# Kernel tuning notes

Measured on AMD Instinct MI355X. Metric: run time of the kernel, lower is better.

The kernel has to match this reference:

```python
import jax, jax.numpy as jnp
import numpy as np
from jax import lax

B, CI, CO, H, W = 2, 256, 256, 128, 128
K = 3
K2 = K * K  # 9 kernel taps
BN_EPS = 1e-5


def setup_inputs() -> dict:
    key = jax.random.key(0)
    ks = jax.random.split(key, 9)
    x = jax.random.normal(ks[0], (B, CI, H, W), jnp.float32)
    # conv_offset_mask: Conv2d(chi, 3*K2, 3, stride=1, pad=1) -> [o_y/o_x interleaved (2*K2) | mask (K2)]
    w_off = jax.random.normal(ks[1], (3 * K2, CI, K, K), jnp.float32) * 0.01
    b_off = jax.random.normal(ks[2], (3 * K2,), jnp.float32) * 0.01
    # modulated deformable conv weight/bias
    w_dcn = jax.random.normal(ks[3], (CO, CI, K, K), jnp.float32) * (1.0 / np.float32(np.sqrt(CI * K2)))
    b_dcn = jax.random.normal(ks[4], (CO,), jnp.float32) * 0.01
    # BatchNorm2d (eval-mode affine + running stats)
    gamma = jax.random.uniform(ks[5], (CO,), jnp.float32, 0.5, 1.5)
    beta = jax.random.normal(ks[6], (CO,), jnp.float32) * 0.1
    run_mean = jax.random.normal(ks[7], (CO,), jnp.float32) * 0.1
    run_var = jax.random.uniform(ks[8], (CO,), jnp.float32, 0.5, 1.5)
    return {"x": x, "w_off": w_off, "b_off": b_off, "w_dcn": w_dcn,
            "b_dcn": b_dcn, "gamma": gamma, "beta": beta,
            "run_mean": run_mean, "run_var": run_var}


def _bilinear(x, py, px):
    """Sample x [B,C,H,W] at fractional coords (py,px) [B,H,W]; zero outside."""
    Bx, C, Hx, Wx = x.shape
    y0 = jnp.floor(py)
    x0 = jnp.floor(px)
    ly = py - y0
    lx = px - x0
    xf = x.reshape(Bx, C, Hx * Wx)

    def gather(yy, xx):
        valid = ((yy >= 0) & (yy <= Hx - 1) & (xx >= 0) & (xx <= Wx - 1)).astype(x.dtype)
        yi = jnp.clip(yy, 0, Hx - 1).astype(jnp.int32)
        xi = jnp.clip(xx, 0, Wx - 1).astype(jnp.int32)
        idx = (yi * Wx + xi).reshape(Bx, 1, Hx * Wx)
        v = jnp.take_along_axis(xf, idx, axis=2).reshape(Bx, C, Hx, Wx)
        return v * valid[:, None]

    w00 = ((1 - ly) * (1 - lx))[:, None]
    w01 = ((1 - ly) * lx)[:, None]
    w10 = (ly * (1 - lx))[:, None]
    w11 = (ly * lx)[:, None]
    return (w00 * gather(y0, x0) + w01 * gather(y0, x0 + 1)
            + w10 * gather(y0 + 1, x0) + w11 * gather(y0 + 1, x0 + 1))


def _deform_conv_bn_relu(x, w_off, b_off, w_dcn, b_dcn, gamma, beta, run_mean, run_var):
    # offset/mask predictor conv (stride 1, pad 1)
    om = lax.conv_general_dilated(x, w_off, (1, 1), ((1, 1), (1, 1))) + b_off[None, :, None, None]
    dy = om[:, 0:2 * K2:2]          # [B,K2,H,W]
    dx = om[:, 1:2 * K2:2]          # [B,K2,H,W]
    mask = jax.nn.sigmoid(om[:, 2 * K2:])  # [B,K2,H,W] modulation

    hh = jnp.arange(H, dtype=x.dtype)[:, None]  # [H,1]
    ww = jnp.arange(W, dtype=x.dtype)[None, :]  # [1,W]

    out = jnp.zeros((x.shape[0], w_dcn.shape[0], H, W), x.dtype)
    for k in range(K2):  # fixed small loop over the 9 kernel taps
        i, j = k // K, k % K
        py = hh - 1 + i + dy[:, k]  # pad=1, dilation=1
        px = ww - 1 + j + dx[:, k]
        val = _bilinear(x, py, px) * mask[:, k][:, None]  # [B,CI,H,W]
        out = out + jnp.einsum('oc,bchw->bohw', w_dcn[:, :, i, j], val)
    out = out + b_dcn[None, :, None, None]

    # BatchNorm2d (eval mode) + ReLU
    inv = gamma / jnp.sqrt(run_var + BN_EPS)
    out = out * inv[None, :, None, None] + (beta - run_mean * inv)[None, :, None, None]
    return jnp.maximum(out, 0.0)


def reference(x, w_off, b_off, w_dcn, b_dcn, gamma, beta, run_mean, run_var):
    return _deform_conv_bn_relu(x, w_off, b_off, w_dcn, b_dcn, gamma, beta, run_mean, run_var)
```

## Files before the change

### kernel.cpp

```cpp
#include <hip/hip_runtime.h>
#include <math.h>

#define Bn 2
#define CIc 256
#define COc 256
#define Hh 128
#define Ww 128
#define HW (Hh*Ww)

typedef unsigned short u16;
typedef unsigned int u32;
typedef __bf16 bf16x8 __attribute__((ext_vector_type(8)));
typedef float  f32x4  __attribute__((ext_vector_type(4)));
typedef float  f32x2  __attribute__((ext_vector_type(2)));
typedef u32    u32x4v __attribute__((ext_vector_type(4)));

#define WOFP_OFF  0
#define WPACK_OFF 36864
#define SCALE_OFF 331776
#define SHIFT_OFF 332032
#define XT_OFF    332288

__device__ __forceinline__ u16 f2bf(float f) {
    u32 u = __builtin_bit_cast(u32, f);
    return (u16)((u + 0x7FFFu + ((u >> 16) & 1u)) >> 16);
}
__device__ __forceinline__ u32 pkbf(float lo, float hi) {
    __bf16 a = (__bf16)lo, b = (__bf16)hi;
    return (u32)__builtin_bit_cast(u16, a) | ((u32)__builtin_bit_cast(u16, b) << 16);
}
__device__ __forceinline__ f32x2 unpk(u32 u) {
    f32x2 r;
    r.x = __builtin_bit_cast(float, u << 16);
    r.y = __builtin_bit_cast(float, u & 0xFFFF0000u);
    return r;
}

__global__ void prep_kernel(const float* __restrict__ w_off,
                            const float* __restrict__ w_dcn,
                            const float* __restrict__ b_dcn,
                            const float* __restrict__ gamma,
                            const float* __restrict__ beta,
                            const float* __restrict__ rmean,
                            const float* __restrict__ rvar,
                            float* __restrict__ ws) {
    int tid = blockIdx.x*blockDim.x + threadIdx.x;
    int nth = gridDim.x*blockDim.x;
    u16* wofp = (u16*)(ws + WOFP_OFF);
    u16* wpk  = (u16*)(ws + WPACK_OFF);
    for (int idx = tid; idx < 9*8*32*4*8; idx += nth) {
        int j = idx & 7, kb = (idx>>3)&3, co = (idx>>5)&31, s = (idx>>10)&7, k = idx>>13;
        int ci = kb*64 + s*8 + j;
        float v = (co < 27) ? w_off[(co*CIc + ci)*9 + k] : 0.f;
        wofp[idx] = f2bf(v);
    }
    for (int idx = tid; idx < 9*8*256*4*8; idx += nth) {
        int j = idx & 7, kb = (idx>>3)&3, co = (idx>>5)&255, s = (idx>>13)&7, k = idx>>16;
        int ci = kb*64 + s*8 + j;
        wpk[idx] = f2bf(w_dcn[(co*CIc + ci)*9 + k]);
    }
    if (tid < COc) {
        float inv = gamma[tid] * rsqrtf(rvar[tid] + 1e-5f);
        ws[SCALE_OFF+tid] = inv;
        ws[SHIFT_OFF+tid] = beta[tid] - rmean[tid]*inv + b_dcn[tid]*inv;
    }
}

__global__ __launch_bounds__(256) void transpose_kernel(const float* __restrict__ x,
                                                        float* __restrict__ ws) {
    __shared__ float tile[256][33];
    int bid = blockIdx.x;
    int b   = bid >> 9;
    int pxt = bid & 511;
    const float* xb = x + (size_t)b*CIc*HW + pxt*32;
    int px = threadIdx.x & 31, cg = threadIdx.x >> 5;
    #pragma unroll 8
    for (int it = 0; it < 32; it++) {
        int ci = it*8 + cg;
        tile[ci][px] = xb[(size_t)ci*HW + px];
    }
    __syncthreads();
    int px2 = threadIdx.x >> 3, oct = threadIdx.x & 7;
    u16* xto = (u16*)(ws + XT_OFF) + (((size_t)b*HW + pxt*32 + px2) << 8);
    #pragma unroll
    for (int uu = 0; uu < 4; uu++) {
        int u = uu*8 + oct;
        int cib = (u & 3)*64 + (u >> 2)*8;
        u32x4v v;
        #pragma unroll
        for (int t = 0; t < 4; t++)
            v[t] = pkbf(tile[cib + 2*t][px2], tile[cib + 2*t + 1][px2]);
        *(u32x4v*)(xto + u*8) = v;
    }
}

__device__ __forceinline__ void calc_corners(const float* spy, const float* spxs, const float* smk,
        int k, int p_s, int sub, const u16* xt,
        float& w00, float& w01, float& w10, float& w11,
        const u16*& x00, const u16*& x01, const u16*& x10, const u16*& x11) {
    float pyv = spy[k*64 + p_s], pxv = spxs[k*64 + p_s], mv = smk[k*64 + p_s];
    float y0f = floorf(pyv), x0f = floorf(pxv);
    float ly = pyv - y0f, lx = pxv - x0f;
    int y0 = (int)y0f, x0i = (int)x0f;
    int y1 = y0 + 1, x1i = x0i + 1;
    float wy0 = ((unsigned)y0  < Hh) ? (1.f-ly) : 0.f;
    float wy1 = ((unsigned)y1  < Hh) ? ly       : 0.f;
    float wx0 = ((unsigned)x0i < Ww) ? (1.f-lx) : 0.f;
    float wx1 = ((unsigned)x1i < Ww) ? lx       : 0.f;
    w00 = wy0*wx0*mv; w01 = wy0*wx1*mv; w10 = wy1*wx0*mv; w11 = wy1*wx1*mv;
    int cy0 = min(max(y0,0),Hh-1), cy1 = min(max(y1,0),Hh-1);
    int cx0 = min(max(x0i,0),Ww-1), cx1 = min(max(x1i,0),Ww-1);
    x00 = xt + ((((cy0<<7)+cx0)<<8) + sub*8);
    x01 = xt + ((((cy0<<7)+cx1)<<8) + sub*8);
    x10 = xt + ((((cy1<<7)+cx0)<<8) + sub*8);
    x11 = xt + ((((cy1<<7)+cx1)<<8) + sub*8);
}

__global__ __launch_bounds__(256, 2) void fused_kernel(const float* __restrict__ b_off,
                                                       const float* __restrict__ ws,
                                                       float* __restrict__ out) {
    __shared__ __align__(16) char smem[65536 + 3*576*4];
    float* fin  = (float*)smem;
    float* spy  = (float*)(smem + 65536);
    float* spxs = spy + 576;
    float* smk  = spxs + 576;

    int tid = threadIdx.x;
    int bid = blockIdx.x;
    int tile = (bid & 7)*64 + (bid >> 3);
    int b = tile >> 8;
    int pixbase = (tile & 255) * 64;
    int h  = pixbase >> 7;
    int w0 = pixbase & 127;

    const u16* wofp = (const u16*)(ws + WOFP_OFF);
    const u16* wpk  = (const u16*)(ws + WPACK_OFF);
    const u16* xt   = (const u16*)(ws + XT_OFF) + (size_t)b*HW*256;

    int l  = tid & 63;
    int wv = tid >> 6;
    int kb = l >> 4;
    int aoff = (l & 15)*32 + kb*8;
    int pxl = l & 15;

    {
        int pxa = wv*16 + (l & 15);
        f32x4 oa0 = {0.f,0.f,0.f,0.f}, oa1 = {0.f,0.f,0.f,0.f};
        #pragma unroll
        for (int k = 0; k < 9; k++) {
            int ky = k/3, kx = k - 3*ky;
            int y  = h + ky - 1;
            int xw = w0 + pxa + kx - 1;
            bool ok = ((unsigned)y < Hh) && ((unsigned)xw < Ww);
            const u16* brow = xt + (((y << 7) + xw) << 8);
            const u16* wk = wofp + k*8192;
            #pragma unroll
            for (int s = 0; s < 8; s++) {
                bf16x8 bf = {};
                if (ok) bf = *(const bf16x8*)(brow + s*32 + kb*8);
                bf16x8 a0 = *(const bf16x8*)(wk + s*1024 + aoff);
                bf16x8 a1 = *(const bf16x8*)(wk + s*1024 + 512 + aoff);
                oa0 = __builtin_amdgcn_mfma_f32_16x16x32_bf16(a0, bf, oa0, 0,0,0);
                oa1 = __builtin_amdgcn_mfma_f32_16x16x32_bf16(a1, bf, oa1, 0,0,0);
            }
        }
        #pragma unroll
        for (int r = 0; r < 4; r++) {
            fin[(kb*4 + r)*64 + pxa]      = oa0[r];
            fin[(16 + kb*4 + r)*64 + pxa] = oa1[r];
        }
    }
    __syncthreads();
    for (int idx = tid; idx < 576; idx += 256) {
        int k = idx >> 6, p = idx & 63;
        float dy = fin[(2*k)*64 + p]   + b_off[2*k];
        float dx = fin[(2*k+1)*64 + p] + b_off[2*k+1];
        float mv = fin[(18+k)*64 + p]  + b_off[18+k];
        spy[idx]  = (float)(h - 1 + k/3) + dy;
        spxs[idx] = (float)(w0 + p - 1 + k%3) + dx;
        smk[idx]  = 1.f/(1.f + __expf(-mv));
    }
    __syncthreads();

    int p_s = tid >> 2;
    int sub = tid & 3;
    u32 wrbase0 = (u32)p_s*512;
    u32 wsub = (u32)sub << 4;
    u32 wswz = (u32)(p_s & 7) << 4;
    u32 rswz = (u32)(pxl & 7) << 4;

    f32x4 acc[4][4];
    #pragma unroll
    for (int mi = 0; mi < 4; mi++)
        #pragma unroll
        for (int bq = 0; bq < 4; bq++)
            acc[mi][bq] = (f32x4){0.f,0.f,0.f,0.f};

    {
        float w00,w01,w10,w11; const u16 *x00,*x01,*x10,*x11;
        calc_corners(spy, spxs, smk, 0, p_s, sub, xt, w00,w01,w10,w11, x00,x01,x10,x11);
        u32x4v g[4][4];
        #pragma unroll
        for (int hh = 0; hh < 2; hh++) {
            #pragma unroll
            for (int it = 0; it < 4; it++) {
                int o = (hh*4 + it) << 5;
                g[it][0] = *(const u32x4v*)(x00 + o);
                g[it][1] = *(const u32x4v*)(x01 + o);
                g[it][2] = *(const u32x4v*)(x10 + o);
                g[it][3] = *(const u32x4v*)(x11 + o);
            }
            #pragma unroll
            for (int it = 0; it < 4; it++) {
                u32x4v vv;
                #pragma unroll
                for (int w2 = 0; w2 < 4; w2++) {
                    f32x2 r = unpk(g[it][0][w2])*w00 + unpk(g[it][1][w2])*w01
                            + unpk(g[it][2][w2])*w10 + unpk(g[it][3][w2])*w11;
                    vv[w2] = pkbf(r.x, r.y);
                }
                u32 uoff = (((u32)(hh*4+it) << 6) | wsub) ^ wswz;
                *(u32x4v*)(smem + wrbase0 + uoff) = vv;
            }
        }
    }
    __syncthreads();

    for (int k = 0; k < 9; k++) {
        const char* base_r = smem + ((k & 1) << 15);
        char* base_w = smem + (((k + 1) & 1) << 15);
        const u16* wkbase = wpk + k*65536 + wv*2048 + aoff;

        float w00,w01,w10,w11; const u16 *x00=xt,*x01=xt,*x10=xt,*x11=xt;
        bool stage = (k != 8);
        if (stage)
            calc_corners(spy, spxs, smk, k+1, p_s, sub, xt, w00,w01,w10,w11, x00,x01,x10,x11);

        u32x4v g[4][4];
        if (stage) {
            #pragma unroll
            for (int it = 0; it < 4; it++) {
                int o = it << 5;
                g[it][0] = *(const u32x4v*)(x00 + o);
                g[it][1] = *(const u32x4v*)(x01 + o);
                g[it][2] = *(const u32x4v*)(x10 + o);
                g[it][3] = *(const u32x4v*)(x11 + o);
            }
        }
        #pragma unroll
        for (int s = 0; s < 4; s++) {
            const u16* wkk = wkbase + s*8192;
            bf16x8 a0 = *(const bf16x8*)(wkk);
            bf16x8 a1 = *(const bf16x8*)(wkk + 512);
            bf16x8 a2 = *(const bf16x8*)(wkk + 1024);
            bf16x8 a3 = *(const bf16x8*)(wkk + 1536);
            u32 inn = ((u32)(s*64 + kb*16)) ^ rswz;
            #pragma unroll
            for (int bq = 0; bq < 4; bq++) {
                bf16x8 bb = *(const bf16x8*)(base_r + (pxl + bq*16)*512 + inn);
                acc[0][bq] = __builtin_amdgcn_mfma_f32_16x16x32_bf16(a0,bb,acc[0][bq],0,0,0);
                acc[1][bq] = __builtin_amdgcn_mfma_f32_16x16x32_bf16(a1,bb,acc[1][bq],0,0,0);
                acc[2][bq] = __builtin_amdgcn_mfma_f32_16x16x32_bf16(a2,bb,acc[2][bq],0,0,0);
                acc[3][bq] = __builtin_amdgcn_mfma_f32_16x16x32_bf16(a3,bb,acc[3][bq],0,0,0);
            }
        }
        if (stage) {
            #pragma unroll
            for (int it = 0; it < 4; it++) {
                u32x4v vv;
                #pragma unroll
                for (int w2 = 0; w2 < 4; w2++) {
                    f32x2 r = unpk(g[it][0][w2])*w00 + unpk(g[it][1][w2])*w01
                            + unpk(g[it][2][w2])*w10 + unpk(g[it][3][w2])*w11;
                    vv[w2] = pkbf(r.x, r.y);
                }
                u32 uoff = (((u32)it << 6) | wsub) ^ wswz;
                *(u32x4v*)(base_w + wrbase0 + uoff) = vv;
            }
            #pragma unroll
            for (int it = 0; it < 4; it++) {
                int o = (4 + it) << 5;
                g[it][0] = *(const u32x4v*)(x00 + o);
                g[it][1] = *(const u32x4v*)(x01 + o);
                g[it][2] = *(const u32x4v*)(x10 + o);
                g[it][3] = *(const u32x4v*)(x11 + o);
            }
        }
        #pragma unroll
        for (int s = 4; s < 8; s++) {
            const u16* wkk = wkbase + s*8192;
            bf16x8 a0 = *(const bf16x8*)(wkk);
            bf16x8 a1 = *(const bf16x8*)(wkk + 512);
            bf16x8 a2 = *(const bf16x8*)(wkk + 1024);
            bf16x8 a3 = *(const bf16x8*)(wkk + 1536);
            u32 inn = ((u32)(s*64 + kb*16)) ^ rswz;
            #pragma unroll
            for (int bq = 0; bq < 4; bq++) {
                bf16x8 bb = *(const bf16x8*)(base_r + (pxl + bq*16)*512 + inn);
                acc[0][bq] = __builtin_amdgcn_mfma_f32_16x16x32_bf16(a0,bb,acc[0][bq],0,0,0);
                acc[1][bq] = __builtin_amdgcn_mfma_f32_16x16x32_bf16(a1,bb,acc[1][bq],0,0,0);
                acc[2][bq] = __builtin_amdgcn_mfma_f32_16x16x32_bf16(a2,bb,acc[2][bq],0,0,0);
                acc[3][bq] = __builtin_amdgcn_mfma_f32_16x16x32_bf16(a3,bb,acc[3][bq],0,0,0);
            }
        }
        if (stage) {
            #pragma unroll
            for (int it = 0; it < 4; it++) {
                u32x4v vv;
                #pragma unroll
                for (int w2 = 0; w2 < 4; w2++) {
                    f32x2 r = unpk(g[it][0][w2])*w00 + unpk(g[it][1][w2])*w01
                            + unpk(g[it][2][w2])*w10 + unpk(g[it][3][w2])*w11;
                    vv[w2] = pkbf(r.x, r.y);
                }
                u32 uoff = (((u32)(4+it) << 6) | wsub) ^ wswz;
                *(u32x4v*)(base_w + wrbase0 + uoff) = vv;
            }
        }
        __syncthreads();
    }

    int rbase = kb*4;
    #pragma unroll
    for (int mi = 0; mi < 4; mi++) {
        #pragma unroll
        for (int r = 0; r < 4; r++) {
            int co = wv*64 + mi*16 + rbase + r;
            float sc = ws[SCALE_OFF+co], sh = ws[SHIFT_OFF+co];
            float* op = out + ((size_t)(b*COc + co))*HW + pixbase + pxl;
            #pragma unroll
            for (int bq = 0; bq < 4; bq++)
                op[bq*16] = fmaxf(acc[mi][bq][r]*sc + sh, 0.f);
        }
    }
}

extern "C" void kernel_launch(void* const* d_in, const int* in_sizes, int n_in,
                              void* d_out, int out_size, void* d_ws, size_t ws_size,
                              hipStream_t stream) {
    const float* x     = (const float*)d_in[0];
    const float* w_off = (const float*)d_in[1];
    const float* b_off = (const float*)d_in[2];
    const float* w_dcn = (const float*)d_in[3];
    const float* b_dcn = (const float*)d_in[4];
    const float* gamma = (const float*)d_in[5];
    const float* beta  = (const float*)d_in[6];
    const float* rmean = (const float*)d_in[7];
    const float* rvar  = (const float*)d_in[8];
    float* out = (float*)d_out;
    float* ws  = (float*)d_ws;

    prep_kernel<<<512, 256, 0, stream>>>(w_off, w_dcn, b_dcn, gamma, beta, rmean, rvar, ws);
    transpose_kernel<<<1024, 256, 0, stream>>>(x, ws);
    fused_kernel<<<512, 256, 0, stream>>>(b_off, ws, out);
}
```

Baseline: 117.8 us.

## Double fused kernel block to 512 threads, halving per-wave output channels

The fused deformable-conv kernel now runs 8 waves per block instead of 4. Each wave owns 32 output channels instead of 64, so the accumulator register footprint halves, and the launch bound is raised to target more resident waves. The offset-predictor MFMA work and the bilinear gather staging are redistributed so each thread samples 4 chunks instead of 8. The staging loads are also no longer interleaved with the MFMA loop; they are all issued before it. This trades software overlap and weight-register reuse for higher occupancy, but the LDS footprint per block is unchanged, which may limit how many blocks actually co-reside.

```diff
diff --git a/kernel.cpp b/kernel.cpp
--- a/kernel.cpp
+++ b/kernel.cpp
@@ -7,6 +7,7 @@
 #define Hh 128
 #define Ww 128
 #define HW (Hh*Ww)
+#define THREADS 512
 
 typedef unsigned short u16;
 typedef unsigned int u32;
@@ -116,7 +117,7 @@
     x11 = xt + ((((cy1<<7)+cx1)<<8) + sub*8);
 }
 
-__global__ __launch_bounds__(256, 2) void fused_kernel(const float* __restrict__ b_off,
+__global__ __launch_bounds__(512, 4) void fused_kernel(const float* __restrict__ b_off,
                                                        const float* __restrict__ ws,
                                                        float* __restrict__ out) {
     __shared__ __align__(16) char smem[65536 + 3*576*4];
@@ -140,12 +141,13 @@
     int l  = tid & 63;
     int wv = tid >> 6;
     int kb = l >> 4;
-    int aoff = (l & 15)*32 + kb*8;
     int pxl = l & 15;
+    int aoff = pxl*32 + kb*8;
 
     {
-        int pxa = wv*16 + (l & 15);
-        f32x4 oa0 = {0.f,0.f,0.f,0.f}, oa1 = {0.f,0.f,0.f,0.f};
+        int pxa = ((wv >> 1) & 3)*16 + pxl;
+        int coh = wv & 1;
+        f32x4 oa = {0.f,0.f,0.f,0.f};
         #pragma unroll
         for (int k = 0; k < 9; k++) {
             int ky = k/3, kx = k - 3*ky;
@@ -153,25 +155,21 @@
             int xw = w0 + pxa + kx - 1;
             bool ok = ((unsigned)y < Hh) && ((unsigned)xw < Ww);
             const u16* brow = xt + (((y << 7) + xw) << 8);
-            const u16* wk = wofp + k*8192;
+            const u16* wk = wofp + k*8192 + coh*512;
             #pragma unroll
             for (int s = 0; s < 8; s++) {
                 bf16x8 bf = {};
                 if (ok) bf = *(const bf16x8*)(brow + s*32 + kb*8);
                 bf16x8 a0 = *(const bf16x8*)(wk + s*1024 + aoff);
-                bf16x8 a1 = *(const bf16x8*)(wk + s*1024 + 512 + aoff);
-                oa0 = __builtin_amdgcn_mfma_f32_16x16x32_bf16(a0, bf, oa0, 0,0,0);
-                oa1 = __builtin_amdgcn_mfma_f32_16x16x32_bf16(a1, bf, oa1, 0,0,0);
-            }
-        }
-        #pragma unroll
-        for (int r = 0; r < 4; r++) {
-            fin[(kb*4 + r)*64 + pxa]      = oa0[r];
-            fin[(16 + kb*4 + r)*64 + pxa] = oa1[r];
-        }
+                oa = __builtin_amdgcn_mfma_f32_16x16x32_bf16(a0, bf, oa, 0,0,0);
+            }
+        }
+        #pragma unroll
+        for (int r = 0; r < 4; r++)
+            fin[(coh*16 + kb*4 + r)*64 + pxa] = oa[r];
     }
     __syncthreads();
-    for (int idx = tid; idx < 576; idx += 256) {
+    for (int idx = tid; idx < 576; idx += THREADS) {
         int k = idx >> 6, p = idx & 63;
         float dy = fin[(2*k)*64 + p]   + b_off[2*k];
         float dx = fin[(2*k+1)*64 + p] + b_off[2*k+1];
@@ -182,16 +180,16 @@
     }
     __syncthreads();
 
-    int p_s = tid >> 2;
-    int sub = tid & 3;
+    int p_s = tid >> 3;
+    int sub = tid & 7;
     u32 wrbase0 = (u32)p_s*512;
     u32 wsub = (u32)sub << 4;
     u32 wswz = (u32)(p_s & 7) << 4;
     u32 rswz = (u32)(pxl & 7) << 4;
 
-    f32x4 acc[4][4];
+    f32x4 acc[2][4];
     #pragma unroll
-    for (int mi = 0; mi < 4; mi++)
+    for (int mi = 0; mi < 2; mi++)
         #pragma unroll
         for (int bq = 0; bq < 4; bq++)
             acc[mi][bq] = (f32x4){0.f,0.f,0.f,0.f};
@@ -201,120 +199,70 @@
         calc_corners(spy, spxs, smk, 0, p_s, sub, xt, w00,w01,w10,w11, x00,x01,x10,x11);
         u32x4v g[4][4];
         #pragma unroll
-        for (int hh = 0; hh < 2; hh++) {
-            #pragma unroll
-            for (int it = 0; it < 4; it++) {
-                int o = (hh*4 + it) << 5;
-                g[it][0] = *(const u32x4v*)(x00 + o);
-                g[it][1] = *(const u32x4v*)(x01 + o);
-                g[it][2] = *(const u32x4v*)(x10 + o);
-                g[it][3] = *(const u32x4v*)(x11 + o);
-            }
-            #pragma unroll
-            for (int it = 0; it < 4; it++) {
+        for (int t = 0; t < 4; t++) {
+            int o = t << 6;
+            g[t][0] = *(const u32x4v*)(x00 + o);
+            g[t][1] = *(const u32x4v*)(x01 + o);
+            g[t][2] = *(const u32x4v*)(x10 + o);
+            g[t][3] = *(const u32x4v*)(x11 + o);
+        }
+        #pragma unroll
+        for (int t = 0; t < 4; t++) {
+            u32x4v vv;
+            #pragma unroll
+            for (int w2 = 0; w2 < 4; w2++) {
+                f32x2 r = unpk(g[t][0][w2])*w00 + unpk(g[t][1][w2])*w01
+                        + unpk(g[t][2][w2])*w10 + unpk(g[t][3][w2])*w11;
+                vv[w2] = pkbf(r.x, r.y);
+            }
+            u32 uoff = (((u32)t << 7) | wsub) ^ wswz;
+            *(u32x4v*)(smem + wrbase0 + uoff) = vv;
+        }
+    }
+    __syncthreads();
+
+    for (int k = 0; k < 9; k++) {
+        const char* base_r = smem + ((k & 1) << 15);
+        char* base_w = smem + (((k + 1) & 1) << 15);
+        const u16* wkbase = wpk + k*65536 + wv*1024 + aoff;
+
+        if (k != 8) {
+            float w00,w01,w10,w11; const u16 *x00,*x01,*x10,*x11;
+            calc_corners(spy, spxs, smk, k+1, p_s, sub, xt, w00,w01,w10,w11, x00,x01,x10,x11);
+            u32x4v g[4][4];
+            #pragma unroll
+            for (int t = 0; t < 4; t++) {
+                int o = t << 6;
+                g[t][0] = *(const u32x4v*)(x00 + o);
+                g[t][1] = *(const u32x4v*)(x01 + o);
+                g[t][2] = *(const u32x4v*)(x10 + o);
+                g[t][3] = *(const u32x4v*)(x11 + o);
+            }
+            #pragma unroll
+            for (int t = 0; t < 4; t++) {
                 u32x4v vv;
                 #pragma unroll
                 for (int w2 = 0; w2 < 4; w2++) {
-                    f32x2 r = unpk(g[it][0][w2])*w00 + unpk(g[it][1][w2])*w01
-                            + unpk(g[it][2][w2])*w10 + unpk(g[it][3][w2])*w11;
+                    f32x2 r = unpk(g[t][0][w2])*w00 + unpk(g[t][1][w2])*w01
+                            + unpk(g[t][2][w2])*w10 + unpk(g[t][3][w2])*w11;
                     vv[w2] = pkbf(r.x, r.y);
                 }
-                u32 uoff = (((u32)(hh*4+it) << 6) | wsub) ^ wswz;
-                *(u32x4v*)(smem + wrbase0 + uoff) = vv;
-            }
-        }
-    }
-    __syncthreads();
-
-    for (int k = 0; k < 9; k++) {
-        const char* base_r = smem + ((k & 1) << 15);
-        char* base_w = smem + (((k + 1) & 1) << 15);
-        const u16* wkbase = wpk + k*65536 + wv*2048 + aoff;
-
-        float w00,w01,w10,w11; const u16 *x00=xt,*x01=xt,*x10=xt,*x11=xt;
-        bool stage = (k != 8);
-        if (stage)
-            calc_corners(spy, spxs, smk, k+1, p_s, sub, xt, w00,w01,w10,w11, x00,x01,x10,x11);
-
-        u32x4v g[4][4];
-        if (stage) {
-            #pragma unroll
-            for (int it = 0; it < 4; it++) {
-                int o = it << 5;
-                g[it][0] = *(const u32x4v*)(x00 + o);
-                g[it][1] = *(const u32x4v*)(x01 + o);
-                g[it][2] = *(const u32x4v*)(x10 + o);
-                g[it][3] = *(const u32x4v*)(x11 + o);
-            }
-        }
-        #pragma unroll
-        for (int s = 0; s < 4; s++) {
+                u32 uoff = (((u32)t << 7) | wsub) ^ wswz;
+                *(u32x4v*)(base_w + wrbase0 + uoff) = vv;
+            }
+        }
+
+        #pragma unroll
+        for (int s = 0; s < 8; s++) {
             const u16* wkk = wkbase + s*8192;
             bf16x8 a0 = *(const bf16x8*)(wkk);
             bf16x8 a1 = *(const bf16x8*)(wkk + 512);
-            bf16x8 a2 = *(const bf16x8*)(wkk + 1024);
-            bf16x8 a3 = *(const bf16x8*)(wkk + 1536);
             u32 inn = ((u32)(s*64 + kb*16)) ^ rswz;
             #pragma unroll
             for (int bq = 0; bq < 4; bq++) {
                 bf16x8 bb = *(const bf16x8*)(base_r + (pxl + bq*16)*512 + inn);
                 acc[0][bq] = __builtin_amdgcn_mfma_f32_16x16x32_bf16(a0,bb,acc[0][bq],0,0,0);
                 acc[1][bq] = __builtin_amdgcn_mfma_f32_16x16x32_bf16(a1,bb,acc[1][bq],0,0,0);
-                acc[2][bq] = __builtin_amdgcn_mfma_f32_16x16x32_bf16(a2,bb,acc[2][bq],0,0,0);
-                acc[3][bq] = __builtin_amdgcn_mfma_f32_16x16x32_bf16(a3,bb,acc[3][bq],0,0,0);
-            }
-        }
-        if (stage) {
-            #pragma unroll
-            for (int it = 0; it < 4; it++) {
-                u32x4v vv;
-                #pragma unroll
-                for (int w2 = 0; w2 < 4; w2++) {
-                    f32x2 r = unpk(g[it][0][w2])*w00 + unpk(g[it][1][w2])*w01
-                            + unpk(g[it][2][w2])*w10 + unpk(g[it][3][w2])*w11;
-                    vv[w2] = pkbf(r.x, r.y);
-                }
-                u32 uoff = (((u32)it << 6) | wsub) ^ wswz;
-                *(u32x4v*)(base_w + wrbase0 + uoff) = vv;
-            }
-            #pragma unroll
-            for (int it = 0; it < 4; it++) {
-                int o = (4 + it) << 5;
-                g[it][0] = *(const u32x4v*)(x00 + o);
-                g[it][1] = *(const u32x4v*)(x01 + o);
-                g[it][2] = *(const u32x4v*)(x10 + o);
-                g[it][3] = *(const u32x4v*)(x11 + o);
-            }
-        }
-        #pragma unroll
-        for (int s = 4; s < 8; s++) {
-            const u16* wkk = wkbase + s*8192;
-            bf16x8 a0 = *(const bf16x8*)(wkk);
-            bf16x8 a1 = *(const bf16x8*)(wkk + 512);
-            bf16x8 a2 = *(const bf16x8*)(wkk + 1024);
-            bf16x8 a3 = *(const bf16x8*)(wkk + 1536);
-            u32 inn = ((u32)(s*64 + kb*16)) ^ rswz;
-            #pragma unroll
-            for (int bq = 0; bq < 4; bq++) {
-                bf16x8 bb = *(const bf16x8*)(base_r + (pxl + bq*16)*512 + inn);
-                acc[0][bq] = __builtin_amdgcn_mfma_f32_16x16x32_bf16(a0,bb,acc[0][bq],0,0,0);
-                acc[1][bq] = __builtin_amdgcn_mfma_f32_16x16x32_bf16(a1,bb,acc[1][bq],0,0,0);
-                acc[2][bq] = __builtin_amdgcn_mfma_f32_16x16x32_bf16(a2,bb,acc[2][bq],0,0,0);
-                acc[3][bq] = __builtin_amdgcn_mfma_f32_16x16x32_bf16(a3,bb,acc[3][bq],0,0,0);
-            }
-        }
-        if (stage) {
-            #pragma unroll
-            for (int it = 0; it < 4; it++) {
-                u32x4v vv;
-                #pragma unroll
-                for (int w2 = 0; w2 < 4; w2++) {
-                    f32x2 r = unpk(g[it][0][w2])*w00 + unpk(g[it][1][w2])*w01
-                            + unpk(g[it][2][w2])*w10 + unpk(g[it][3][w2])*w11;
-                    vv[w2] = pkbf(r.x, r.y);
-                }
-                u32 uoff = (((u32)(4+it) << 6) | wsub) ^ wswz;
-                *(u32x4v*)(base_w + wrbase0 + uoff) = vv;
             }
         }
         __syncthreads();
@@ -322,10 +270,10 @@
 
     int rbase = kb*4;
     #pragma unroll
-    for (int mi = 0; mi < 4; mi++) {
+    for (int mi = 0; mi < 2; mi++) {
         #pragma unroll
         for (int r = 0; r < 4; r++) {
-            int co = wv*64 + mi*16 + rbase + r;
+            int co = wv*32 + mi*16 + rbase + r;
             float sc = ws[SCALE_OFF+co], sh = ws[SHIFT_OFF+co];
             float* op = out + ((size_t)(b*COc + co))*HW + pixbase + pxl;
             #pragma unroll
@@ -352,5 +300,5 @@
 
     prep_kernel<<<512, 256, 0, stream>>>(w_off, w_dcn, b_dcn, gamma, beta, rmean, rvar, ws);
     transpose_kernel<<<1024, 256, 0, stream>>>(x, ws);
-    fused_kernel<<<512, 256, 0, stream>>>(b_off, ws, out);
-}
+    fused_kernel<<<512, 512, 0, stream>>>(b_off, ws, out);
+}
```

New measurement: 127.9 us. 1.09x slower.
